# Optimization experiments

Measured on AMD Instinct MI355X. Metric: run time of the kernel, lower is better.

Reference implementation:

```python
import jax, jax.numpy as jnp
import numpy as np

RCUT = 6.0
EPS = 1e-6
NUM_BASIS = 8
P = 6  # PolynomialSmooth envelope power
N_NODES = 100000
N_EDGES = 3200000
N_GRAPHS = 16

# 27 periodic image shifts: all integer combos of [-1,0,1]^3
_PERIODIC = jnp.asarray(
    np.stack(np.meshgrid(*([[-1, 0, 1]] * 3), indexing='ij'), -1).reshape(27, 3).astype(np.float32)
)


def _sh_lmax2(u):
    """e3nn spherical harmonics, lmax=2, normalize=True, normalization='component'.
    u: [E,3] unit vectors -> [E,9]."""
    x, y, z = u[..., 0], u[..., 1], u[..., 2]
    s3 = jnp.sqrt(jnp.asarray(3.0, u.dtype))
    s5 = jnp.sqrt(jnp.asarray(5.0, u.dtype))
    s15 = jnp.sqrt(jnp.asarray(15.0, u.dtype))
    return jnp.stack([
        jnp.ones_like(x),                      # l=0
        s3 * x, s3 * y, s3 * z,                # l=1
        s15 * x * z,                           # l=2
        s15 * x * y,
        s5 * (y * y - 0.5 * (x * x + z * z)),
        s15 * y * z,
        0.5 * s15 * (z * z - x * x),
    ], axis=-1)


def _bessel(lengths):
    # lengths: [E,1] -> [E,NUM_BASIS]
    k = jnp.arange(1, NUM_BASIS + 1, dtype=lengths.dtype) * jnp.pi / RCUT
    safe = jnp.clip(lengths, EPS, RCUT)
    return jnp.sin(safe * k) / (2.0 * safe)


def _poly_smooth(lengths):
    # standard polynomial envelope (DimeNet-style), zero at r=rcut
    x = jnp.clip(lengths / RCUT, 0.0, 1.0)
    c1 = (P + 1) * (P + 2) / 2.0
    c2 = float(P * (P + 2))
    c3 = P * (P + 1) / 2.0
    xp = x ** P
    return 1.0 - c1 * xp + c2 * xp * x - c3 * xp * x * x


def setup_inputs() -> dict:
    key = jax.random.key(0)
    k1, k2, k3, k4, k5 = jax.random.split(key, 5)
    pos = jax.random.normal(k1, (N_NODES, 3), dtype=jnp.float32) * 5.0
    cells = jax.random.normal(k2, (N_GRAPHS, 3, 3), dtype=jnp.float32)
    edge_index = jax.random.randint(k3, (2, N_EDGES), 0, N_NODES)
    periodic_index = jax.random.randint(k4, (N_EDGES,), 0, 27)
    batch = jnp.sort(jax.random.randint(k5, (N_NODES,), 0, N_GRAPHS))
    return {"pos": pos, "cells": cells, "edge_index": edge_index,
            "periodic_index": periodic_index, "batch": batch}


def reference(pos, cells, edge_index, periodic_index, batch):
    node_src, node_dst = edge_index[0], edge_index[1]
    vectors = pos[node_dst] - pos[node_src]                     # [E,3]
    shifts = _PERIODIC[periodic_index]                          # [E,3]
    src_cells = cells[batch[node_src]]                          # [E,3,3]
    vectors = vectors - jnp.einsum('eij,ei->ej', src_cells, shifts)
    vectors = -vectors                                          # dst == 'atom'
    lengths = jnp.linalg.norm(vectors, axis=-1, keepdims=True)  # [E,1]
    unit = vectors / jnp.maximum(lengths, EPS)                  # normalize=True
    attr = _sh_lmax2(unit)                                      # [E,9]
    basis = _bessel(lengths)                                    # [E,8]
    cutoff = _poly_smooth(lengths)                              # [E,1]
    basis_weight = basis * cutoff                               # [E,8]
    # pack (length, sh attr, smooth, basis_weight) -> [E,19]
    return jnp.concatenate([lengths, attr, cutoff, basis_weight], axis=-1)
```

## Files before the change

kernel.cpp:

```cpp
#include <hip/hip_runtime.h>

#define BLOCK 256
#define WPB (BLOCK / 64)
#define WREG (64 * 19)

typedef float vf4 __attribute__((ext_vector_type(4)));

extern "C" __global__ void __launch_bounds__(BLOCK) pack_pos_batch(
    const float* __restrict__ pos,
    const int*  __restrict__ batch,
    vf4* __restrict__ pos4,
    int N)
{
    const int i = blockIdx.x * BLOCK + threadIdx.x;
    if (i < N) {
        vf4 v;
        v.x = pos[3 * i + 0];
        v.y = pos[3 * i + 1];
        v.z = pos[3 * i + 2];
        v.w = __int_as_float(batch[i]);
        pos4[i] = v;
    }
}

template <bool PACKED>
__global__ void __launch_bounds__(BLOCK) edge_encoding_kernel(
    const float* __restrict__ pos,
    const vf4*   __restrict__ pos4,
    const float* __restrict__ cells,
    const int*   __restrict__ eidx,
    const int*   __restrict__ pidx,
    const int*   __restrict__ batch,
    float* __restrict__ out,
    int E)
{
    __shared__ vf4 s_t[16 * 27];
    __shared__ __align__(64) float s_out[WPB * WREG];

    const int tid = threadIdx.x;
    for (int c = tid; c < 16 * 27; c += BLOCK) {
        const int g = c / 27, p = c % 27;
        const float f0 = (float)(p / 9 - 1);
        const float f1 = (float)((p / 3) % 3 - 1);
        const float f2 = (float)(p % 3 - 1);
        const float* C = cells + g * 9;
        vf4 t;
        t.x = C[0]*f0 + C[3]*f1 + C[6]*f2;
        t.y = C[1]*f0 + C[4]*f1 + C[7]*f2;
        t.z = C[2]*f0 + C[5]*f1 + C[8]*f2;
        t.w = 0.0f;
        s_t[c] = t;
    }
    __syncthreads();

    const int lane = tid & 63;
    const int wid  = tid >> 6;
    const long long e0 = ((long long)blockIdx.x * WPB + wid) * 64;
    if (e0 >= E) return;

    long long e = e0 + lane;
    if (e >= E) e = E - 1;
    const int src = __builtin_nontemporal_load(eidx + e);
    const int dst = __builtin_nontemporal_load(eidx + E + e);
    const int p   = __builtin_nontemporal_load(pidx + e);

    vf4 ps, pd;
    if (PACKED) {
        ps = pos4[src];
        pd = pos4[dst];
    } else {
        ps.x = pos[3*src+0]; ps.y = pos[3*src+1]; ps.z = pos[3*src+2];
        ps.w = __int_as_float(batch[src]);
        pd.x = pos[3*dst+0]; pd.y = pos[3*dst+1]; pd.z = pos[3*dst+2];
        pd.w = 0.0f;
    }

    const float s3  = 1.7320508075688772f;
    const float s5  = 2.2360679774997896f;
    const float s15 = 3.872983346207417f;

    float row[19];
    {
        const int g = __float_as_int(ps.w);
        const vf4 t = s_t[g * 27 + p];

        const float vx = ps.x - pd.x + t.x;
        const float vy = ps.y - pd.y + t.y;
        const float vz = ps.z - pd.z + t.z;

        const float len  = sqrtf(vx*vx + vy*vy + vz*vz);
        const float invl = __builtin_amdgcn_rcpf(fmaxf(len, 1e-6f));
        const float x = vx * invl, y = vy * invl, z = vz * invl;

        row[0] = len;
        row[1] = 1.0f;
        row[2] = s3 * x;
        row[3] = s3 * y;
        row[4] = s3 * z;
        row[5] = s15 * x * z;
        row[6] = s15 * x * y;
        row[7] = s5  * (y*y - 0.5f*(x*x + z*z));
        row[8] = s15 * y * z;
        row[9] = 0.5f * s15 * (z*z - x*x);

        const float xc = fminf(len * (1.0f/6.0f), 1.0f);
        const float x3 = xc * xc * xc;
        const float x6 = x3 * x3;
        const float cut = fmaf(x6, fmaf(xc, fmaf(-21.0f, xc, 48.0f), -28.0f), 1.0f);
        row[10] = cut;

        const float safe = fminf(fmaxf(len, 1e-6f), 6.0f);
        const float a = safe * 0.5235987755982988f;
        const float sa = __sinf(a);
        const float ca = __cosf(a);
        const float w = cut * 0.5f * __builtin_amdgcn_rcpf(safe);
        const float two_ca = 2.0f * ca;
        float s_prev = 0.0f, s_cur = sa;
        row[11] = s_cur * w;
        #pragma unroll
        for (int n = 2; n <= 8; ++n) {
            const float s_next = two_ca * s_cur - s_prev;
            s_prev = s_cur;
            s_cur  = s_next;
            row[10 + n] = s_cur * w;
        }
    }

    float* s_buf = s_out + wid * WREG;
    #pragma unroll
    for (int j = 0; j < 19; ++j) s_buf[lane * 19 + j] = row[j];

    const int nvalid = (int)(((long long)E - e0) < 64 ? (E - e0) : 64);
    float* gout = out + e0 * 19;
    if (nvalid == 64) {
        const vf4* s4 = reinterpret_cast<const vf4*>(s_buf);
        vf4* g4 = reinterpret_cast<vf4*>(gout);
        #pragma unroll
        for (int i = lane; i < 304; i += 64)
            g4[i] = s4[i];
    } else {
        const int nf = nvalid * 19;
        for (int i = lane; i < nf; i += 64)
            gout[i] = s_buf[i];
    }
}

extern "C" void kernel_launch(void* const* d_in, const int* in_sizes, int n_in,
                              void* d_out, int out_size, void* d_ws, size_t ws_size,
                              hipStream_t stream) {
    const float* pos   = (const float*)d_in[0];
    const float* cells = (const float*)d_in[1];
    const int*   eidx  = (const int*)d_in[2];
    const int*   pidx  = (const int*)d_in[3];
    const int*   batch = (const int*)d_in[4];
    float* out = (float*)d_out;

    const int E = in_sizes[3];
    const int N = in_sizes[4];
    const int grid = (int)(((long long)E + BLOCK - 1) / BLOCK);

    if (d_ws != nullptr && ws_size >= (size_t)N * sizeof(vf4)) {
        vf4* pos4 = (vf4*)d_ws;
        const int pgrid = (N + BLOCK - 1) / BLOCK;
        pack_pos_batch<<<pgrid, BLOCK, 0, stream>>>(pos, batch, pos4, N);
        edge_encoding_kernel<true><<<grid, BLOCK, 0, stream>>>(
            pos, pos4, cells, eidx, pidx, batch, out, E);
    } else {
        edge_encoding_kernel<false><<<grid, BLOCK, 0, stream>>>(
            pos, nullptr, cells, eidx, pidx, batch, out, E);
    }
}
```

Before: 326.3 us.

## Make edge kernel persistent with software-pipelined index loads and gathers

Turns the one-tile-per-wave edge kernel into a grid-stride persistent kernel capped at 2048 blocks. Each wave prefetches indices two tiles ahead and gathers node positions one tile ahead, so memory latency overlaps with compute. The precomputed 16x27 shift table is dropped and the periodic shift is recomputed per edge from the cell matrices kept in shared memory. The launch bound now asks for 8 blocks per CU. This trades occupancy-based latency hiding for explicit prefetch, and the extra live registers and per-edge shift math could limit the benefit.

```diff
diff --git a/kernel.cpp b/kernel.cpp
--- a/kernel.cpp
+++ b/kernel.cpp
@@ -1,8 +1,9 @@
 #include <hip/hip_runtime.h>
 
 #define BLOCK 256
-#define WPB (BLOCK / 64)
-#define WREG (64 * 19)
+#define WPB 4
+#define TILE_E 64
+#define WREG (TILE_E * 19)
 
 typedef float vf4 __attribute__((ext_vector_type(4)));
 
@@ -24,7 +25,7 @@
 }
 
 template <bool PACKED>
-__global__ void __launch_bounds__(BLOCK) edge_encoding_kernel(
+__global__ void __launch_bounds__(BLOCK, 8) edge_encoding_kernel(
     const float* __restrict__ pos,
     const vf4*   __restrict__ pos4,
     const float* __restrict__ cells,
@@ -34,114 +35,135 @@
     float* __restrict__ out,
     int E)
 {
-    __shared__ vf4 s_t[16 * 27];
+    __shared__ float s_cells[144];
     __shared__ __align__(64) float s_out[WPB * WREG];
 
     const int tid = threadIdx.x;
-    for (int c = tid; c < 16 * 27; c += BLOCK) {
-        const int g = c / 27, p = c % 27;
-        const float f0 = (float)(p / 9 - 1);
-        const float f1 = (float)((p / 3) % 3 - 1);
-        const float f2 = (float)(p % 3 - 1);
-        const float* C = cells + g * 9;
-        vf4 t;
-        t.x = C[0]*f0 + C[3]*f1 + C[6]*f2;
-        t.y = C[1]*f0 + C[4]*f1 + C[7]*f2;
-        t.z = C[2]*f0 + C[5]*f1 + C[8]*f2;
-        t.w = 0.0f;
-        s_t[c] = t;
-    }
+    if (tid < 144) s_cells[tid] = cells[tid];
     __syncthreads();
 
     const int lane = tid & 63;
     const int wid  = tid >> 6;
-    const long long e0 = ((long long)blockIdx.x * WPB + wid) * 64;
-    if (e0 >= E) return;
+    float* s_buf = s_out + wid * WREG;
 
-    long long e = e0 + lane;
-    if (e >= E) e = E - 1;
-    const int src = __builtin_nontemporal_load(eidx + e);
-    const int dst = __builtin_nontemporal_load(eidx + E + e);
-    const int p   = __builtin_nontemporal_load(pidx + e);
-
-    vf4 ps, pd;
-    if (PACKED) {
-        ps = pos4[src];
-        pd = pos4[dst];
-    } else {
-        ps.x = pos[3*src+0]; ps.y = pos[3*src+1]; ps.z = pos[3*src+2];
-        ps.w = __int_as_float(batch[src]);
-        pd.x = pos[3*dst+0]; pd.y = pos[3*dst+1]; pd.z = pos[3*dst+2];
-        pd.w = 0.0f;
-    }
+    const int ntiles = (E + TILE_E - 1) / TILE_E;
+    const int nwaves = gridDim.x * WPB;
+    int t = blockIdx.x * WPB + wid;
+    if (t >= ntiles) return;
 
     const float s3  = 1.7320508075688772f;
     const float s5  = 2.2360679774997896f;
     const float s15 = 3.872983346207417f;
 
-    float row[19];
-    {
-        const int g = __float_as_int(ps.w);
-        const vf4 t = s_t[g * 27 + p];
+    int s0, d0, p0, s1, d1, p1;
+    vf4 a0, b0;
 
-        const float vx = ps.x - pd.x + t.x;
-        const float vy = ps.y - pd.y + t.y;
-        const float vz = ps.z - pd.z + t.z;
+    auto load_idx = [&](int tt, int& s, int& d, int& p) {
+        if (tt < ntiles) {
+            long long e = (long long)tt * TILE_E + lane;
+            if (e >= E) e = E - 1;
+            s = __builtin_nontemporal_load(eidx + e);
+            d = __builtin_nontemporal_load(eidx + E + e);
+            p = __builtin_nontemporal_load(pidx + e);
+        } else { s = 0; d = 0; p = 13; }
+    };
+    auto do_gather = [&](int s, int d, vf4& a, vf4& b) {
+        if (PACKED) {
+            a = pos4[s];
+            b = pos4[d];
+        } else {
+            a.x = pos[3*s+0]; a.y = pos[3*s+1]; a.z = pos[3*s+2];
+            a.w = __int_as_float(batch[s]);
+            b.x = pos[3*d+0]; b.y = pos[3*d+1]; b.z = pos[3*d+2];
+            b.w = 0.0f;
+        }
+    };
 
-        const float len  = sqrtf(vx*vx + vy*vy + vz*vz);
-        const float invl = __builtin_amdgcn_rcpf(fmaxf(len, 1e-6f));
-        const float x = vx * invl, y = vy * invl, z = vz * invl;
+    load_idx(t, s0, d0, p0);
+    do_gather(s0, d0, a0, b0);
+    load_idx(t + nwaves, s1, d1, p1);
 
-        row[0] = len;
-        row[1] = 1.0f;
-        row[2] = s3 * x;
-        row[3] = s3 * y;
-        row[4] = s3 * z;
-        row[5] = s15 * x * z;
-        row[6] = s15 * x * y;
-        row[7] = s5  * (y*y - 0.5f*(x*x + z*z));
-        row[8] = s15 * y * z;
-        row[9] = 0.5f * s15 * (z*z - x*x);
+    for (; t < ntiles; t += nwaves) {
+        vf4 a1, b1;
+        do_gather(s1, d1, a1, b1);
+        int s2, d2, p2;
+        load_idx(t + 2 * nwaves, s2, d2, p2);
 
-        const float xc = fminf(len * (1.0f/6.0f), 1.0f);
-        const float x3 = xc * xc * xc;
-        const float x6 = x3 * x3;
-        const float cut = fmaf(x6, fmaf(xc, fmaf(-21.0f, xc, 48.0f), -28.0f), 1.0f);
-        row[10] = cut;
+        float row[19];
+        {
+            const int g = __float_as_int(a0.w);
+            const int p = p0;
+            const float f0 = (float)(p / 9 - 1);
+            const float f1 = (float)((p / 3) % 3 - 1);
+            const float f2 = (float)(p % 3 - 1);
 
-        const float safe = fminf(fmaxf(len, 1e-6f), 6.0f);
-        const float a = safe * 0.5235987755982988f;
-        const float sa = __sinf(a);
-        const float ca = __cosf(a);
-        const float w = cut * 0.5f * __builtin_amdgcn_rcpf(safe);
-        const float two_ca = 2.0f * ca;
-        float s_prev = 0.0f, s_cur = sa;
-        row[11] = s_cur * w;
+            const float* C = s_cells + g * 9;
+            const float tx = C[0]*f0 + C[3]*f1 + C[6]*f2;
+            const float ty = C[1]*f0 + C[4]*f1 + C[7]*f2;
+            const float tz = C[2]*f0 + C[5]*f1 + C[8]*f2;
+
+            const float vx = a0.x - b0.x + tx;
+            const float vy = a0.y - b0.y + ty;
+            const float vz = a0.z - b0.z + tz;
+
+            const float len  = sqrtf(vx*vx + vy*vy + vz*vz);
+            const float invl = __builtin_amdgcn_rcpf(fmaxf(len, 1e-6f));
+            const float x = vx * invl, y = vy * invl, z = vz * invl;
+
+            row[0] = len;
+            row[1] = 1.0f;
+            row[2] = s3 * x;
+            row[3] = s3 * y;
+            row[4] = s3 * z;
+            row[5] = s15 * x * z;
+            row[6] = s15 * x * y;
+            row[7] = s5  * (y*y - 0.5f*(x*x + z*z));
+            row[8] = s15 * y * z;
+            row[9] = 0.5f * s15 * (z*z - x*x);
+
+            const float xc = fminf(len * (1.0f/6.0f), 1.0f);
+            const float x3 = xc * xc * xc;
+            const float x6 = x3 * x3;
+            const float cut = fmaf(x6, fmaf(xc, fmaf(-21.0f, xc, 48.0f), -28.0f), 1.0f);
+            row[10] = cut;
+
+            const float safe = fminf(fmaxf(len, 1e-6f), 6.0f);
+            const float a = safe * 0.5235987755982988f;
+            const float sa = __sinf(a);
+            const float ca = __cosf(a);
+            const float w = cut * 0.5f * __builtin_amdgcn_rcpf(safe);
+            const float two_ca = 2.0f * ca;
+            float s_prev = 0.0f, s_cur = sa;
+            row[11] = s_cur * w;
+            #pragma unroll
+            for (int n = 2; n <= 8; ++n) {
+                const float s_next = two_ca * s_cur - s_prev;
+                s_prev = s_cur;
+                s_cur  = s_next;
+                row[10 + n] = s_cur * w;
+            }
+        }
+
         #pragma unroll
-        for (int n = 2; n <= 8; ++n) {
-            const float s_next = two_ca * s_cur - s_prev;
-            s_prev = s_cur;
-            s_cur  = s_next;
-            row[10 + n] = s_cur * w;
+        for (int j = 0; j < 19; ++j) s_buf[lane * 19 + j] = row[j];
+
+        const long long e0 = (long long)t * TILE_E;
+        const int nvalid = (int)(((long long)E - e0) < TILE_E ? (E - e0) : TILE_E);
+        float* gout = out + e0 * 19;
+        if (nvalid == TILE_E) {
+            const vf4* s4 = reinterpret_cast<const vf4*>(s_buf);
+            vf4* g4 = reinterpret_cast<vf4*>(gout);
+            #pragma unroll
+            for (int i = lane; i < 304; i += 64)
+                g4[i] = s4[i];
+        } else {
+            const int nf = nvalid * 19;
+            for (int i = lane; i < nf; i += 64)
+                gout[i] = s_buf[i];
         }
-    }
 
-    float* s_buf = s_out + wid * WREG;
-    #pragma unroll
-    for (int j = 0; j < 19; ++j) s_buf[lane * 19 + j] = row[j];
-
-    const int nvalid = (int)(((long long)E - e0) < 64 ? (E - e0) : 64);
-    float* gout = out + e0 * 19;
-    if (nvalid == 64) {
-        const vf4* s4 = reinterpret_cast<const vf4*>(s_buf);
-        vf4* g4 = reinterpret_cast<vf4*>(gout);
-        #pragma unroll
-        for (int i = lane; i < 304; i += 64)
-            g4[i] = s4[i];
-    } else {
-        const int nf = nvalid * 19;
-        for (int i = lane; i < nf; i += 64)
-            gout[i] = s_buf[i];
+        a0 = a1; b0 = b1; p0 = p1;
+        s1 = s2; d1 = d2; p1 = p2;
     }
 }
 
@@ -157,7 +179,9 @@
 
     const int E = in_sizes[3];
     const int N = in_sizes[4];
-    const int grid = (int)(((long long)E + BLOCK - 1) / BLOCK);
+    const int ntiles = (E + TILE_E - 1) / TILE_E;
+    int grid = (ntiles + WPB - 1) / WPB;
+    if (grid > 2048) grid = 2048;
 
     if (d_ws != nullptr && ws_size >= (size_t)N * sizeof(vf4)) {
         vf4* pos4 = (vf4*)d_ws;
```

Result: no change. 324.0 us (-0.7%).
